# Performance work log

Measured on AMD Instinct MI355X. Metric: run time of the kernel, lower is better.

The kernel has to match this reference:

```python
import jax, jax.numpy as jnp
import numpy as np


def setup_inputs() -> dict:
    key = jax.random.key(0)
    k1, k2, k3 = jax.random.split(key, 3)
    B, S, D = 2, 2048, 1024
    N_COMPRESS, RANK = 64, 64
    x = jax.random.normal(k1, (B, S, D), dtype=jnp.float32)
    router_w = jax.random.normal(k2, (N_COMPRESS, D), dtype=jnp.float32) * (1.0 / np.sqrt(D))
    # compress neurons (orthogonal-init in torch; gaussian scaled is fine for a numeric baseline)
    neurons = jax.random.normal(k3, (N_COMPRESS, D, RANK), dtype=jnp.float32) * (1.0 / np.sqrt(D))
    return {"x": x, "router_w": router_w, "neurons": neurons}


TOP_K = 2


def reference(x, router_w, neurons):
    # x: [B,S,D], router_w: [N,D], neurons: [N,D,R]
    B, S, D = x.shape
    R = neurons.shape[-1]
    scores = jnp.einsum('bsd,nd->bsn', x, router_w)            # [B,S,N]
    topk_scores, topk_idx = jax.lax.top_k(scores, TOP_K)       # [B,S,K]
    topk_weights = jax.nn.softmax(topk_scores, axis=-1)        # [B,S,K]
    output = jnp.zeros((B, S, R), dtype=x.dtype)
    for i in range(TOP_K):  # small fixed loop, mirrors original slot-wise combine
        idx = topk_idx[:, :, i]                                # [B,S]
        sel = neurons[idx]                                     # [B,S,D,R] gather
        proj = jnp.einsum('bsd,bsdr->bsr', x, sel)             # per-token matvec
        output = output + topk_weights[:, :, i:i + 1] * proj
    return output, topk_idx, topk_weights
```

## Files before the change

kernel.cpp:

```cpp
#include <hip/hip_runtime.h>
#include <hip/hip_bf16.h>


typedef unsigned short u16;
typedef unsigned int u32;
typedef __attribute__((ext_vector_type(8))) short short8;
typedef __attribute__((ext_vector_type(4))) float f32x4;

__device__ __forceinline__ float bf2f(u16 u) {
    u32 v = ((u32)u) << 16; float f; __builtin_memcpy(&f, &v, 4); return f;
}
__device__ __forceinline__ u16 f2bf(float f) {
    u32 u; __builtin_memcpy(&u, &f, 4);
    u32 r = u + 0x7fff + ((u >> 16) & 1);
    return (u16)(r >> 16);
}
__device__ __forceinline__ u32 pack2(float a, float b) {
    return ((u32)f2bf(b) << 16) | (u32)f2bf(a);
}

#define T_TOKENS 4096
#define DDIM 1024
#define NEXP 64
#define RDIM 64
#define LCAP 1024
#define OUT_IDX_OFF 262144
#define OUT_W_OFF 270336

struct LdBF {
    const u16* p;
    __device__ __forceinline__ float4 ld4(size_t i) const {
        ushort4 v = *(const ushort4*)(p + i);
        return make_float4(bf2f(v.x), bf2f(v.y), bf2f(v.z), bf2f(v.w));
    }
    __device__ __forceinline__ float ld1(size_t i) const { return bf2f(p[i]); }
};
struct LdF32 {
    const float* p;
    __device__ __forceinline__ float4 ld4(size_t i) const { return *(const float4*)(p + i); }
    __device__ __forceinline__ float ld1(size_t i) const { return p[i]; }
};

__device__ __forceinline__ int detect_f32(const u16* x, int* lds_cnt) {
    if (threadIdx.x == 0) *lds_cnt = 0;
    __syncthreads();
    if (threadIdx.x < 256) {
        unsigned e = (x[threadIdx.x] >> 7) & 0xFF;
        if (e >= 0x68 && e <= 0x88) atomicAdd(lds_cnt, 1);
    }
    __syncthreads();
    int f = (*lds_cnt < 200) ? 1 : 0;
    __syncthreads();
    return f;
}

template <class LD>
__device__ __forceinline__ void score_body(LD xld, LD rwld,
                                           float* xs , float* wt ,
                                           float* sc , float* Sb, u16* xbf) {
    const int tid = threadIdx.x;
    const int g = blockIdx.x >> 1;
    const int kh = blockIdx.x & 1;
    const size_t t0 = (size_t)g * 8;
    const int kbase = kh * 512;
    const int wv = tid >> 6;
    const int lane = tid & 63;
    const int tg = lane & 1;
    const int eg = (lane >> 1) & 7;
    const int kql = (lane >> 4) & 3;
    const int dd = 4 * kql + 16 * wv;
    const int kc0 = blockIdx.x & 7;

    const int sm = tid >> 4;
    const int sd4 = (tid & 15) * 4;

    float acc[4][8];
#pragma unroll
    for (int mi = 0; mi < 4; ++mi)
#pragma unroll
        for (int ei = 0; ei < 8; ++ei) acc[mi][ei] = 0.f;

    float4 px;
    if (tid < 128) px = xld.ld4((t0 + sm) * DDIM + kbase + kc0 * 64 + sd4);
    float4 pw[4];
#pragma unroll
    for (int h = 0; h < 4; ++h) {
        int i4 = tid + h * 256;
        pw[h] = rwld.ld4((size_t)(i4 >> 4) * DDIM + kbase + kc0 * 64 + (i4 & 15) * 4);
    }

    for (int i = 0; i < 8; ++i) {
        if (i > 0) __syncthreads();
        if (tid < 128) {
            *(float4*)&xs[sm * 68 + sd4] = px;
            int kchn = kbase + ((i + kc0) & 7) * 64;
            uint2 b;
            b.x = pack2(px.x, px.y);
            b.y = pack2(px.z, px.w);
            *(uint2*)&xbf[(t0 + sm) * DDIM + kchn + sd4] = b;
        }
#pragma unroll
        for (int h = 0; h < 4; ++h) {
            int i4 = tid + h * 256;
            *(float4*)&wt[(i4 >> 4) * 68 + (i4 & 15) * 4] = pw[h];
        }
        __syncthreads();

        if (i < 7) {
            int kn = kbase + ((i + 1 + kc0) & 7) * 64;
            if (tid < 128) px = xld.ld4((t0 + sm) * DDIM + kn + sd4);
#pragma unroll
            for (int h = 0; h < 4; ++h) {
                int i4 = tid + h * 256;
                pw[h] = rwld.ld4((size_t)(i4 >> 4) * DDIM + kn + (i4 & 15) * 4);
            }
        }

        float4 xv[4], wv4[8];
#pragma unroll
        for (int mi = 0; mi < 4; ++mi)
            xv[mi] = *(const float4*)&xs[(tg + 2 * mi) * 68 + dd];
#pragma unroll
        for (int ei = 0; ei < 8; ++ei)
            wv4[ei] = *(const float4*)&wt[(eg + 8 * ei) * 68 + dd];
#pragma unroll
        for (int mi = 0; mi < 4; ++mi)
#pragma unroll
            for (int ei = 0; ei < 8; ++ei)
                acc[mi][ei] += xv[mi].x * wv4[ei].x + xv[mi].y * wv4[ei].y +
                               xv[mi].z * wv4[ei].z + xv[mi].w * wv4[ei].w;
    }

#pragma unroll
    for (int mi = 0; mi < 4; ++mi)
#pragma unroll
        for (int ei = 0; ei < 8; ++ei) {
            float v = acc[mi][ei];
            v += __shfl_xor(v, 16, 64);
            v += __shfl_xor(v, 32, 64);
            acc[mi][ei] = v;
        }
    __syncthreads();

    for (int w = 0; w < 4; ++w) {
        if (wv == w && kql == 0) {
#pragma unroll
            for (int mi = 0; mi < 4; ++mi)
#pragma unroll
                for (int ei = 0; ei < 8; ++ei) {
                    int idx = (tg + 2 * mi) * 65 + eg + 8 * ei;
                    sc[idx] = (w == 0) ? acc[mi][ei] : sc[idx] + acc[mi][ei];
                }
        }
        __syncthreads();
    }

    if (tid < 128) {
        int t = tid >> 4, e4 = (tid & 15) * 4;
        const float* s = &sc[t * 65 + e4];
        float4 v = make_float4(s[0], s[1], s[2], s[3]);
        *(float4*)&Sb[((size_t)kh * T_TOKENS + t0 + t) * 64 + e4] = v;
    }
}

__global__ __launch_bounds__(256, 4) void score_part(const void* x, const void* rw,
                                                     float* Sb, int* wsCnt, u16* xbf) {
    __shared__ float xs[8 * 68];
    __shared__ float wt[64 * 68];
    __shared__ float sc[8 * 65];
    __shared__ int dc;
    if (blockIdx.x == 0 && threadIdx.x < NEXP) wsCnt[threadIdx.x] = 0;
    int f = detect_f32((const u16*)x, &dc);
    if (f)
        score_body(LdF32{(const float*)x}, LdF32{(const float*)rw}, xs, wt, sc, Sb, xbf);
    else
        score_body(LdBF{(const u16*)x}, LdBF{(const u16*)rw}, xs, wt, sc, Sb, xbf);
}

__global__ __launch_bounds__(64) void topk_softmax(const float* Sb, float* out,
                                                   float* wsW, int* wsCnt,
                                                   int* wsList) {
    int t = blockIdx.x * 64 + threadIdx.x;
    const float* s0 = Sb + (size_t)t * 64;
    const float* s1 = Sb + ((size_t)T_TOKENS + t) * 64;
    float best = -1e30f, secv = -1e30f;
    int bi = 0, si = 0;
    for (int j = 0; j < NEXP; j += 4) {
        float4 a = *(const float4*)(s0 + j);
        float4 b = *(const float4*)(s1 + j);
        float v0 = a.x + b.x, v1 = a.y + b.y, v2 = a.z + b.z, v3 = a.w + b.w;
        if (v0 > best) { secv = best; si = bi; best = v0; bi = j; }
        else if (v0 > secv) { secv = v0; si = j; }
        if (v1 > best) { secv = best; si = bi; best = v1; bi = j + 1; }
        else if (v1 > secv) { secv = v1; si = j + 1; }
        if (v2 > best) { secv = best; si = bi; best = v2; bi = j + 2; }
        else if (v2 > secv) { secv = v2; si = j + 2; }
        if (v3 > best) { secv = best; si = bi; best = v3; bi = j + 3; }
        else if (v3 > secv) { secv = v3; si = j + 3; }
    }
    float w0 = 1.0f / (1.0f + expf(secv - best));
    float w1 = 1.0f - w0;
    out[OUT_IDX_OFF + (size_t)t * 2 + 0] = (float)bi;
    out[OUT_IDX_OFF + (size_t)t * 2 + 1] = (float)si;
    out[OUT_W_OFF + (size_t)t * 2 + 0] = w0;
    out[OUT_W_OFF + (size_t)t * 2 + 1] = w1;
    wsW[t * 2 + 0] = w0;
    wsW[t * 2 + 1] = w1;
    int p0 = atomicAdd(&wsCnt[bi], 1);
    if (p0 < LCAP) wsList[bi * LCAP + p0] = t * 2 + 0;
    int p1 = atomicAdd(&wsCnt[si], 1);
    if (p1 < LCAP) wsList[si * LCAP + p1] = t * 2 + 1;
}

template <class LD>
__device__ __forceinline__ void egemm_body(LD nld, const u16* xbf,
                                           const int* wsCnt, const int* wsList,
                                           float* P,
                                           u16* Ab , u16* Bb ,
                                           int* eL ) {
    const int tid = threadIdx.x;
    const int e = blockIdx.x >> 3;
    const int oct = blockIdx.x & 7;
    const int cntE = min(wsCnt[e], LCAP);
    if (cntE <= 0) return;
    const int wv = tid >> 6;
    const int lane = tid & 63;
    const int l15 = lane & 15, quad = lane >> 4;
    const size_t nbase = (size_t)e * (DDIM * RDIM);
    const int k0 = oct * 128;

    for (int j = tid; j < cntE; j += 256) eL[j] = wsList[e * LCAP + j];

    {
        const int rq = tid & 15;
        const int kpB = tid >> 4;
        u32* bb = (u32*)Bb;
#pragma unroll
        for (int h = 0; h < 4; ++h) {
            int kp = kpB + h * 16;
            float4 g0 = nld.ld4(nbase + (size_t)(k0 + 2 * kp) * RDIM + rq * 4);
            float4 g1 = nld.ld4(nbase + (size_t)(k0 + 2 * kp + 1) * RDIM + rq * 4);
            bb[(rq * 4 + 0) * 68 + kp] = pack2(g0.x, g1.x);
            bb[(rq * 4 + 1) * 68 + kp] = pack2(g0.y, g1.y);
            bb[(rq * 4 + 2) * 68 + kp] = pack2(g0.z, g1.z);
            bb[(rq * 4 + 3) * 68 + kp] = pack2(g0.w, g1.w);
        }
    }
    __syncthreads();

    const int rowA = tid >> 4;
    const int kqA = tid & 15;
    const int ntiles = (cntE + 15) >> 4;

    uint4 ca, na;
    {
        int t2r = eL[min(rowA, cntE - 1)];
        ca = *(const uint4*)&xbf[(size_t)(t2r >> 1) * DDIM + k0 + kqA * 8];
    }
    na = ca;
    if (ntiles > 1) {
        int t2r = eL[min(16 + rowA, cntE - 1)];
        na = *(const uint4*)&xbf[(size_t)(t2r >> 1) * DDIM + k0 + kqA * 8];
    }

    for (int ti = 0; ti < ntiles; ++ti) {
        const int base = ti * 16;
        const int valid = min(16, cntE - base);
        if (ti > 0) __syncthreads();
        *(uint4*)&((u32*)Ab)[rowA * 68 + kqA * 4] = ca;
        __syncthreads();
        if (ti + 2 < ntiles) {
            int t2r = eL[min(base + 32 + rowA, cntE - 1)];
            ca = *(const uint4*)&xbf[(size_t)(t2r >> 1) * DDIM + k0 + kqA * 8];
        }

        f32x4 acc = {0.f, 0.f, 0.f, 0.f};
#pragma unroll
        for (int ko = 0; ko < 4; ++ko) {
            int kofs = ko * 32 + quad * 8;
            short8 bfr = *(const short8*)&Bb[(16 * wv + l15) * 136 + kofs];
            short8 af = *(const short8*)&Ab[l15 * 136 + kofs];
            acc = __builtin_amdgcn_mfma_f32_16x16x32_bf16(af, bfr, acc, 0, 0, 0);
        }

#pragma unroll
        for (int reg = 0; reg < 4; ++reg) {
            int m = quad * 4 + reg;
            if (m < valid) {
                int t2 = eL[base + m];
                P[(size_t)t2 * 512 + oct * 64 + 16 * wv + l15] = acc[reg];
            }
        }

        uint4 s = ca;
        ca = na;
        na = s;
    }
}

__global__ __launch_bounds__(256, 2) void expert_gemm(const void* x, const void* neurons,
                                                      const u16* xbf,
                                                      const int* wsCnt, const int* wsList,
                                                      float* P) {
    __shared__ u16 Ab[16 * 136];
    __shared__ u16 Bb[64 * 136];
    __shared__ int eL[LCAP];
    __shared__ int dc;
    int f = detect_f32((const u16*)x, &dc);
    if (f)
        egemm_body(LdF32{(const float*)neurons}, xbf, wsCnt, wsList, P, Ab, Bb, eL);
    else
        egemm_body(LdBF{(const u16*)neurons}, xbf, wsCnt, wsList, P, Ab, Bb, eL);
}

__global__ __launch_bounds__(256) void combine(const float* P, const float* wsW,
                                               float* out) {
    int i = blockIdx.x * 256 + threadIdx.x;
    int t = i >> 6, r = i & 63;
    const float* p0 = P + (size_t)(2 * t) * 512 + r;
    const float* p1 = P + (size_t)(2 * t + 1) * 512 + r;
    float s0 = 0.f, s1 = 0.f;
#pragma unroll
    for (int o = 0; o < 8; ++o) {
        s0 += p0[o * 64];
        s1 += p1[o * 64];
    }
    out[i] = wsW[2 * t] * s0 + wsW[2 * t + 1] * s1;
}

extern "C" void kernel_launch(void* const* d_in, const int* in_sizes, int n_in,
                              void* d_out, int out_size, void* d_ws, size_t ws_size,
                              hipStream_t stream) {
    const void* x = d_in[0];
    const void* rw = d_in[1];
    const void* neurons = d_in[2];
    float* out = (float*)d_out;

    char* wsc = (char*)d_ws;
    float* wsW = (float*)wsc;
    int* wsCnt = (int*)(wsc + 32 * 1024);
    int* wsList = (int*)(wsc + 32 * 1024 + 256);
    float* Sb = (float*)(wsc + (1 << 20));
    float* P = (float*)(wsc + (4 << 20));
    u16* xbf = (u16*)(wsc + (24 << 20));

    score_part<<<1024, 256, 0, stream>>>(x, rw, Sb, wsCnt, xbf);
    topk_softmax<<<64, 64, 0, stream>>>(Sb, out, wsW, wsCnt, wsList);
    expert_gemm<<<512, 256, 0, stream>>>(x, neurons, xbf, wsCnt, wsList, P);
    combine<<<1024, 256, 0, stream>>>(P, wsW, out);
}
```

Before: 122.3 us.

## Precompute packed bf16 neuron slabs in score kernel for expert GEMM

Adds extra blocks to the scoring kernel that convert each expert's neuron slice into the packed bf16, transposed shared-memory layout and store it to workspace. The expert GEMM then bulk-copies the ready slab into shared memory instead of loading, converting and scattering f32 neurons itself. This moves conversion work off the critical expert GEMM and lets it run alongside routing. The cost is an extra global write and read of the converted slabs and a larger scoring grid.

```diff
diff --git a/kernel.cpp b/kernel.cpp
--- a/kernel.cpp
+++ b/kernel.cpp
@@ -26,6 +26,7 @@
 #define LCAP 1024
 #define OUT_IDX_OFF 262144
 #define OUT_W_OFF 270336
+#define SLAB_U32 4352
 
 struct LdBF {
     const u16* p;
@@ -52,6 +53,31 @@
     int f = (*lds_cnt < 200) ? 1 : 0;
     __syncthreads();
     return f;
+}
+
+template <class LD>
+__device__ __forceinline__ void conv_body(LD nld, int cb, u32* bb ,
+                                          u32* nbf) {
+    const int tid = threadIdx.x;
+    const int e = cb >> 3;
+    const int oct = cb & 7;
+    const size_t nbase = (size_t)e * (DDIM * RDIM);
+    const int k0 = oct * 128;
+    const int rq = tid & 15;
+    const int kpB = tid >> 4;
+#pragma unroll
+    for (int h = 0; h < 4; ++h) {
+        int kp = kpB + h * 16;
+        float4 g0 = nld.ld4(nbase + (size_t)(k0 + 2 * kp) * RDIM + rq * 4);
+        float4 g1 = nld.ld4(nbase + (size_t)(k0 + 2 * kp + 1) * RDIM + rq * 4);
+        bb[(rq * 4 + 0) * 68 + kp] = pack2(g0.x, g1.x);
+        bb[(rq * 4 + 1) * 68 + kp] = pack2(g0.y, g1.y);
+        bb[(rq * 4 + 2) * 68 + kp] = pack2(g0.z, g1.z);
+        bb[(rq * 4 + 3) * 68 + kp] = pack2(g0.w, g1.w);
+    }
+    __syncthreads();
+    u32* dst = nbf + (size_t)cb * SLAB_U32;
+    for (int i = tid; i < SLAB_U32; i += 256) dst[i] = bb[i];
 }
 
 template <class LD>
@@ -164,13 +190,23 @@
 }
 
 __global__ __launch_bounds__(256, 4) void score_part(const void* x, const void* rw,
-                                                     float* Sb, int* wsCnt, u16* xbf) {
+                                                     const void* neurons,
+                                                     float* Sb, int* wsCnt, u16* xbf,
+                                                     u32* nbf) {
     __shared__ float xs[8 * 68];
-    __shared__ float wt[64 * 68];
+    __shared__ __align__(16) float wt[64 * 68];
     __shared__ float sc[8 * 65];
     __shared__ int dc;
     if (blockIdx.x == 0 && threadIdx.x < NEXP) wsCnt[threadIdx.x] = 0;
     int f = detect_f32((const u16*)x, &dc);
+    if (blockIdx.x >= 1024) {
+        int cb = blockIdx.x - 1024;
+        if (f)
+            conv_body(LdF32{(const float*)neurons}, cb, (u32*)wt, nbf);
+        else
+            conv_body(LdBF{(const u16*)neurons}, cb, (u32*)wt, nbf);
+        return;
+    }
     if (f)
         score_body(LdF32{(const float*)x}, LdF32{(const float*)rw}, xs, wt, sc, Sb, xbf);
     else
@@ -212,12 +248,12 @@
     if (p1 < LCAP) wsList[si * LCAP + p1] = t * 2 + 1;
 }
 
-template <class LD>
-__device__ __forceinline__ void egemm_body(LD nld, const u16* xbf,
-                                           const int* wsCnt, const int* wsList,
-                                           float* P,
-                                           u16* Ab , u16* Bb ,
-                                           int* eL ) {
+__global__ __launch_bounds__(256, 2) void expert_gemm(const u16* xbf, const u32* nbf,
+                                                      const int* wsCnt, const int* wsList,
+                                                      float* P) {
+    __shared__ __align__(16) u16 Ab[16 * 136];
+    __shared__ __align__(16) u16 Bb[64 * 136];
+    __shared__ int eL[LCAP];
     const int tid = threadIdx.x;
     const int e = blockIdx.x >> 3;
     const int oct = blockIdx.x & 7;
@@ -226,25 +262,14 @@
     const int wv = tid >> 6;
     const int lane = tid & 63;
     const int l15 = lane & 15, quad = lane >> 4;
-    const size_t nbase = (size_t)e * (DDIM * RDIM);
     const int k0 = oct * 128;
 
     for (int j = tid; j < cntE; j += 256) eL[j] = wsList[e * LCAP + j];
 
     {
-        const int rq = tid & 15;
-        const int kpB = tid >> 4;
-        u32* bb = (u32*)Bb;
-#pragma unroll
-        for (int h = 0; h < 4; ++h) {
-            int kp = kpB + h * 16;
-            float4 g0 = nld.ld4(nbase + (size_t)(k0 + 2 * kp) * RDIM + rq * 4);
-            float4 g1 = nld.ld4(nbase + (size_t)(k0 + 2 * kp + 1) * RDIM + rq * 4);
-            bb[(rq * 4 + 0) * 68 + kp] = pack2(g0.x, g1.x);
-            bb[(rq * 4 + 1) * 68 + kp] = pack2(g0.y, g1.y);
-            bb[(rq * 4 + 2) * 68 + kp] = pack2(g0.z, g1.z);
-            bb[(rq * 4 + 3) * 68 + kp] = pack2(g0.w, g1.w);
-        }
+        const uint4* src = (const uint4*)(nbf + (size_t)blockIdx.x * SLAB_U32);
+        uint4* dst = (uint4*)Bb;
+        for (int i = tid; i < SLAB_U32 / 4; i += 256) dst[i] = src[i];
     }
     __syncthreads();
 
@@ -298,21 +323,6 @@
     }
 }
 
-__global__ __launch_bounds__(256, 2) void expert_gemm(const void* x, const void* neurons,
-                                                      const u16* xbf,
-                                                      const int* wsCnt, const int* wsList,
-                                                      float* P) {
-    __shared__ u16 Ab[16 * 136];
-    __shared__ u16 Bb[64 * 136];
-    __shared__ int eL[LCAP];
-    __shared__ int dc;
-    int f = detect_f32((const u16*)x, &dc);
-    if (f)
-        egemm_body(LdF32{(const float*)neurons}, xbf, wsCnt, wsList, P, Ab, Bb, eL);
-    else
-        egemm_body(LdBF{(const u16*)neurons}, xbf, wsCnt, wsList, P, Ab, Bb, eL);
-}
-
 __global__ __launch_bounds__(256) void combine(const float* P, const float* wsW,
                                                float* out) {
     int i = blockIdx.x * 256 + threadIdx.x;
@@ -343,9 +353,10 @@
     float* Sb = (float*)(wsc + (1 << 20));
     float* P = (float*)(wsc + (4 << 20));
     u16* xbf = (u16*)(wsc + (24 << 20));
-
-    score_part<<<1024, 256, 0, stream>>>(x, rw, Sb, wsCnt, xbf);
+    u32* nbf = (u32*)(wsc + (40 << 20));
+
+    score_part<<<1536, 256, 0, stream>>>(x, rw, neurons, Sb, wsCnt, xbf, nbf);
     topk_softmax<<<64, 64, 0, stream>>>(Sb, out, wsW, wsCnt, wsList);
-    expert_gemm<<<512, 256, 0, stream>>>(x, neurons, xbf, wsCnt, wsList, P);
+    expert_gemm<<<512, 256, 0, stream>>>(xbf, nbf, wsCnt, wsList, P);
     combine<<<1024, 256, 0, stream>>>(P, wsW, out);
 }
```

After: 122.4 us. Within noise of the previous version (+0.1%).
